# Optimization experiments

Hardware: AMD Instinct MI355X
Metric: run time of the kernel (lower is better)

## Reference

```python
import jax, jax.numpy as jnp
import numpy as np

CHANNELS = 32
HIDDEN = 1024
LAYERS = 8
NODE_TYPES = 7
N_NODES = 500_000
N_EDGES = 2_000_000
NUM_GRAPHS = 1024


def setup_inputs() -> dict:
    key = jax.random.key(0)
    ks = jax.random.split(key, 8)
    nodes = jax.random.randint(ks[0], (N_NODES,), 0, NODE_TYPES)
    sources = jax.random.randint(ks[1], (N_EDGES,), 0, N_NODES)
    targets = jax.random.randint(ks[2], (N_EDGES,), 0, N_NODES)
    # sorted graph ids covering all NUM_GRAPHS graphs (no empty graphs)
    batch = (jnp.arange(N_NODES) * NUM_GRAPHS) // N_NODES
    emb = jax.random.normal(ks[3], (NODE_TYPES, CHANNELS), dtype=jnp.float32)
    # xavier-normal-ish init for the 8 layers x {out, back} 32x32 convs
    xavier_std = (2.0 / (CHANNELS + CHANNELS)) ** 0.5
    conv_w = jax.random.normal(ks[4], (LAYERS, 2, CHANNELS, CHANNELS), dtype=jnp.float32) * xavier_std
    hidden_w = jax.random.normal(ks[5], (CHANNELS, HIDDEN), dtype=jnp.float32) * 0.05
    hidden_b = jax.random.normal(ks[6], (HIDDEN,), dtype=jnp.float32) * 0.05
    out_w = jax.random.normal(ks[7], (HIDDEN, 1), dtype=jnp.float32) * 0.05
    return dict(nodes=nodes, sources=sources, targets=targets, batch=batch,
                emb=emb, conv_w=conv_w, hidden_w=hidden_w, hidden_b=hidden_b,
                out_w=out_w)


def reference(nodes, sources, targets, batch, emb, conv_w, hidden_w, hidden_b, out_w):
    n = nodes.shape[0]
    ones_e = jnp.ones(sources.shape[0], dtype=jnp.float32)
    # norm = 1 / (1 + in-degree), norm_t = 1 / (1 + out-degree)  [N,1]
    norm = (1.0 / (1.0 + jax.ops.segment_sum(ones_e, targets, num_segments=n)))[:, None]
    norm_t = (1.0 / (1.0 + jax.ops.segment_sum(ones_e, sources, num_segments=n)))[:, None]
    node_counts = jax.ops.segment_sum(jnp.ones(n, dtype=jnp.float32), batch,
                                      num_segments=NUM_GRAPHS)

    x = emb[nodes]  # [N, C]

    def conv(x, s, t, nrm, w):
        # x.index_add(0, t, x[s]) -> x + scatter_add of gathered source feats
        agg = nrm * (x + jax.ops.segment_sum(x[s], t, num_segments=n))
        return jax.nn.relu(agg @ w)

    for l in range(LAYERS):
        x = x + conv(x, sources, targets, norm, conv_w[l, 0]) \
              + conv(x, targets, sources, norm_t, conv_w[l, 1])

    # mean pooling per graph
    g = jax.ops.segment_sum(x, batch, num_segments=NUM_GRAPHS) / node_counts[:, None]
    h = jax.nn.relu(g @ hidden_w + hidden_b)
    return (h @ out_w).squeeze(-1)  # [NUM_GRAPHS]
```

## Files before the change

kernel.cpp:

```cpp
#include <hip/hip_runtime.h>

#define CHANNELS 32
#define HIDDEN 1024
#define LAYERS 8
#define NRANGE 8

typedef __attribute__((ext_vector_type(8))) short short8;
typedef __attribute__((ext_vector_type(4))) float float4v;

__device__ __forceinline__ short f2bf_rne(float f) {
    union { float f; unsigned u; } v; v.f = f;
    unsigned r = v.u + 0x7fffu + ((v.u >> 16) & 1u);
    return (short)(r >> 16);
}
__device__ __forceinline__ float bf2f(short h) {
    union { float f; unsigned u; } v; v.u = ((unsigned)(unsigned short)h) << 16;
    return v.f;
}
__device__ __forceinline__ float bfu2f(unsigned short h) {
    union { float f; unsigned u; } v; v.u = ((unsigned)h) << 16;
    return v.f;
}


__global__ __launch_bounds__(256)
void pre_kernel(const int* __restrict__ src, const int* __restrict__ tgt,
                int* __restrict__ deg2,
                const int* __restrict__ nodes, const float* __restrict__ emb,
                unsigned short* __restrict__ hi0, unsigned short* __restrict__ lo,
                const int* __restrict__ batch, float* __restrict__ counts,
                int n_nodes, int n_edges, int n_graphs, int rsh,
                int degB, int initB) {
    int bid = blockIdx.x;
    int tid = threadIdx.x;
    if (bid < degB) {
        int r = bid & (NRANGE - 1);
        int chunk = bid >> 3;
        int base = chunk * 2048;
#pragma unroll
        for (int j = 0; j < 8; j++) {
            int e = base + j * 256 + tid;
            if (e < n_edges) {
                int t = __builtin_nontemporal_load(tgt + e);
                int s = __builtin_nontemporal_load(src + e);
                if ((t >> rsh) == r) atomicAdd(&deg2[t], 1);
                if ((s >> rsh) == r) atomicAdd(&deg2[n_nodes + s], 1);
            }
        }
    } else if (bid < degB + initB) {
        int gid = (bid - degB) * 256 + tid;
        int i = gid >> 5, c = gid & 31;
        if (i < n_nodes) {
            float v = emb[nodes[i] * CHANNELS + c];
            short h = f2bf_rne(v);
            hi0[gid] = (unsigned short)h;
            lo[gid]  = (unsigned short)f2bf_rne(v - bf2f(h));
        }
    } else {
        int b = (bid - degB - initB) * 256 + tid;
        if (b < n_graphs) {
            int lo_i = 0, hi_i = n_nodes;
            while (lo_i < hi_i) { int mid = (lo_i + hi_i) >> 1; if (batch[mid] < b) lo_i = mid + 1; else hi_i = mid; }
            int s0 = lo_i;
            lo_i = 0; hi_i = n_nodes;
            while (lo_i < hi_i) { int mid = (lo_i + hi_i) >> 1; if (batch[mid] < b + 1) lo_i = mid + 1; else hi_i = mid; }
            counts[b] = (float)(lo_i - s0);
        }
    }
}


__global__ __launch_bounds__(256)
void scan_pass1(const int* __restrict__ deg, int* __restrict__ bs, int n) {
    __shared__ int sh[256];
    int t = threadIdx.x;
    int base = blockIdx.x * 2048 + t * 8;
    int s = 0;
#pragma unroll
    for (int j = 0; j < 8; j++) { int idx = base + j; if (idx < n) s += deg[idx]; }
    sh[t] = s; __syncthreads();
    for (int st = 128; st > 0; st >>= 1) { if (t < st) sh[t] += sh[t + st]; __syncthreads(); }
    if (t == 0) bs[blockIdx.x] = sh[0];
}

__global__ void scan_pass2(int* __restrict__ bs, int nb) {
    __shared__ int sh[1024];
    int t = threadIdx.x;
    int v = (t < nb) ? bs[t] : 0;
    sh[t] = v; __syncthreads();
    for (int off = 1; off < 1024; off <<= 1) {
        int u = (t >= off) ? sh[t - off] : 0; __syncthreads();
        sh[t] += u; __syncthreads();
    }
    if (t < nb) bs[t] = sh[t] - v;
}

__global__ __launch_bounds__(256)
void scan_pass3(const int* __restrict__ deg, const int* __restrict__ bs,
                int* __restrict__ off, int n) {
    __shared__ int sh[256];
    int t = threadIdx.x;
    int base = blockIdx.x * 2048 + t * 8;
    int v[8]; int s = 0;
#pragma unroll
    for (int j = 0; j < 8; j++) { int idx = base + j; v[j] = (idx < n) ? deg[idx] : 0; s += v[j]; }
    sh[t] = s; __syncthreads();
    for (int st = 1; st < 256; st <<= 1) {
        int u = (t >= st) ? sh[t - st] : 0; __syncthreads();
        sh[t] += u; __syncthreads();
    }
    int acc = bs[blockIdx.x] + sh[t] - s;
#pragma unroll
    for (int j = 0; j < 8; j++) { int idx = base + j; if (idx < n) off[idx] = acc; acc += v[j]; }
}


__global__ __launch_bounds__(256)
void scatter_range_kernel(const int* __restrict__ src, const int* __restrict__ tgt,
                          int* __restrict__ cur2, int* __restrict__ nbr,
                          int n_nodes, int n_edges, int rsh, int rbase) {
    int r = rbase + (blockIdx.x & (NRANGE - 1));
    int chunk = blockIdx.x >> 3;
    int base = chunk * 2048;
#pragma unroll
    for (int j = 0; j < 8; j++) {
        int e = base + j * 256 + threadIdx.x;
        if (e < n_edges) {
            int t = __builtin_nontemporal_load(tgt + e);
            int s = __builtin_nontemporal_load(src + e);
            if ((t >> rsh) == r) { int p = atomicAdd(&cur2[t], 1);           nbr[p] = s; }
            if ((s >> rsh) == r) { int q = atomicAdd(&cur2[n_nodes + s], 1); nbr[q] = t; }
        }
    }
}


__global__ __launch_bounds__(256, 8)
void layer_mfma(const int* __restrict__ off2, const int* __restrict__ nbr,
                const float* __restrict__ wbase,
                const unsigned short* __restrict__ hi_in,
                unsigned short* __restrict__ hi_out,
                unsigned short* __restrict__ lo,
                int n_nodes, int n_edges) {
    __shared__ short A1h[64][32], A2h[64][32];
    __shared__ short W0h[32][32], W1h[32][32];
    __shared__ int offIn[65], offOut[65];

    int tid = threadIdx.x;
    int nodeblock = blockIdx.x * 64;

    for (int idx = tid; idx < CHANNELS * CHANNELS; idx += 256) {
        int k = idx >> 5, n = idx & 31;
        W0h[n][k] = f2bf_rne(wbase[idx]);
        W1h[n][k] = f2bf_rne(wbase[CHANNELS * CHANNELS + idx]);
    }
    if (tid < 65) {
        int idx = nodeblock + tid;
        offIn[tid]  = (idx <= n_nodes) ? off2[idx] : n_edges;
        int idx2 = n_nodes + idx;
        offOut[tid] = (idx2 < 2 * n_nodes) ? off2[idx2] : 2 * n_edges;
    }
    __syncthreads();

    int c = tid & 31, g = tid >> 5;

    int bi_c, d1_c, bo_c, d2_c, nbl1_c, nbl2_c, node_c;
    float xv_c;
    {
        int local = g;
        node_c = nodeblock + local;
        bi_c = offIn[local];  d1_c = offIn[local + 1] - bi_c;
        bo_c = offOut[local]; d2_c = offOut[local + 1] - bo_c;
        nbl1_c = (c < d1_c) ? nbr[bi_c + c] : 0;
        nbl2_c = (c < d2_c) ? nbr[bo_c + c] : 0;
        xv_c = (node_c < n_nodes)
             ? bfu2f(hi_in[node_c * CHANNELS + c]) + bfu2f(lo[node_c * CHANNELS + c]) : 0.f;
    }

    for (int pass = 0; pass < 8; pass++) {
        int bi_n = 0, d1_n = 0, bo_n = 0, d2_n = 0, nbl1_n = 0, nbl2_n = 0, node_n = 0;
        float xv_n = 0.f;
        if (pass < 7) {
            int local = (pass + 1) * 8 + g;
            node_n = nodeblock + local;
            bi_n = offIn[local];  d1_n = offIn[local + 1] - bi_n;
            bo_n = offOut[local]; d2_n = offOut[local + 1] - bo_n;
            nbl1_n = (c < d1_n) ? nbr[bi_n + c] : 0;
            nbl2_n = (c < d2_n) ? nbr[bo_n + c] : 0;
            xv_n = (node_n < n_nodes)
                 ? bfu2f(hi_in[node_n * CHANNELS + c]) + bfu2f(lo[node_n * CHANNELS + c]) : 0.f;
        }

        int local = pass * 8 + g;
        int i = node_c;
        int self = (i < n_nodes) ? i : 0;

        int m1 = d1_c < 32 ? d1_c : 32;
        int m2 = d2_c < 32 ? d2_c : 32;
        int mm = m1 > m2 ? m1 : m2;

        float a1 = 0.f, a2 = 0.f;
        for (int j = 0; j < mm; j += 4) {
            int p0 = __shfl(nbl1_c, (j)     & 31, 32);
            int p1 = __shfl(nbl1_c, (j + 1) & 31, 32);
            int p2 = __shfl(nbl1_c, (j + 2) & 31, 32);
            int p3 = __shfl(nbl1_c, (j + 3) & 31, 32);
            int q0 = __shfl(nbl2_c, (j)     & 31, 32);
            int q1 = __shfl(nbl2_c, (j + 1) & 31, 32);
            int q2 = __shfl(nbl2_c, (j + 2) & 31, 32);
            int q3 = __shfl(nbl2_c, (j + 3) & 31, 32);
            p0 = (j     < m1) ? p0 : self;
            p1 = (j + 1 < m1) ? p1 : self;
            p2 = (j + 2 < m1) ? p2 : self;
            p3 = (j + 3 < m1) ? p3 : self;
            q0 = (j     < m2) ? q0 : self;
            q1 = (j + 1 < m2) ? q1 : self;
            q2 = (j + 2 < m2) ? q2 : self;
            q3 = (j + 3 < m2) ? q3 : self;
            float u0 = bfu2f(hi_in[p0 * CHANNELS + c]);
            float u1 = bfu2f(hi_in[p1 * CHANNELS + c]);
            float u2 = bfu2f(hi_in[p2 * CHANNELS + c]);
            float u3 = bfu2f(hi_in[p3 * CHANNELS + c]);
            float w0 = bfu2f(hi_in[q0 * CHANNELS + c]);
            float w1 = bfu2f(hi_in[q1 * CHANNELS + c]);
            float w2 = bfu2f(hi_in[q2 * CHANNELS + c]);
            float w3 = bfu2f(hi_in[q3 * CHANNELS + c]);
            a1 += (j     < m1) ? u0 : 0.f;
            a1 += (j + 1 < m1) ? u1 : 0.f;
            a1 += (j + 2 < m1) ? u2 : 0.f;
            a1 += (j + 3 < m1) ? u3 : 0.f;
            a2 += (j     < m2) ? w0 : 0.f;
            a2 += (j + 1 < m2) ? w1 : 0.f;
            a2 += (j + 2 < m2) ? w2 : 0.f;
            a2 += (j + 3 < m2) ? w3 : 0.f;
        }
        for (int e = bi_c + 32; e < bi_c + d1_c; e++) a1 += bfu2f(hi_in[nbr[e] * CHANNELS + c]);
        for (int e = bo_c + 32; e < bo_c + d2_c; e++) a2 += bfu2f(hi_in[nbr[e] * CHANNELS + c]);

        if (i < n_nodes) {
            float n1 = 1.0f / (1.0f + (float)d1_c);
            float n2 = 1.0f / (1.0f + (float)d2_c);
            a1 = n1 * (xv_c + a1);
            a2 = n2 * (xv_c + a2);
            A1h[local][c] = f2bf_rne(a1);
            A2h[local][c] = f2bf_rne(a2);
        } else {
            A1h[local][c] = 0;
            A2h[local][c] = 0;
        }

        bi_c = bi_n; d1_c = d1_n; bo_c = bo_n; d2_c = d2_n;
        nbl1_c = nbl1_n; nbl2_c = nbl2_n; xv_c = xv_n; node_c = node_n;
    }
    __syncthreads();

    int wv = tid >> 6, lane = tid & 63;
    int m = lane & 15, quad = lane >> 4;
    int row0 = wv * 16;

    short8 a1h = *(const short8*)&A1h[row0 + m][quad * 8];
    short8 a2h = *(const short8*)&A2h[row0 + m][quad * 8];

    float4v dd[4];
#pragma unroll
    for (int h = 0; h < 2; h++) {
        int n0 = h * 16 + m;
        short8 b0h = *(const short8*)&W0h[n0][quad * 8];
        short8 b1h = *(const short8*)&W1h[n0][quad * 8];
        float4v d1 = {0.f, 0.f, 0.f, 0.f};
        d1 = __builtin_amdgcn_mfma_f32_16x16x32_bf16(a1h, b0h, d1, 0, 0, 0);
        float4v d2 = {0.f, 0.f, 0.f, 0.f};
        d2 = __builtin_amdgcn_mfma_f32_16x16x32_bf16(a2h, b1h, d2, 0, 0, 0);
        dd[h * 2] = d1; dd[h * 2 + 1] = d2;
    }

#pragma unroll
    for (int h = 0; h < 2; h++) {
        float4v d1 = dd[h * 2], d2 = dd[h * 2 + 1];
#pragma unroll
        for (int r = 0; r < 4; r++) {
            int local = row0 + quad * 4 + r;
            int node = nodeblock + local;
            if (node < n_nodes) {
                int col = h * 16 + m;
                size_t idx = (size_t)node * CHANNELS + col;
                float base = bfu2f(hi_in[idx]) + bfu2f(lo[idx]);
                float v = base + fmaxf(d1[r], 0.f) + fmaxf(d2[r], 0.f);
                short hn = f2bf_rne(v);
                hi_out[idx] = (unsigned short)hn;
                lo[idx]     = (unsigned short)f2bf_rne(v - bf2f(hn));
            }
        }
    }
}


#define POOL_CHUNK 2048

__global__ __launch_bounds__(256)
void pool_kernel(const int* __restrict__ batch,
                 const unsigned short* __restrict__ hi,
                 const unsigned short* __restrict__ lo,
                 float* __restrict__ g, int n_nodes) {
    int c = threadIdx.x & 31;
    int r = threadIdx.x >> 5;
    int base = blockIdx.x * POOL_CHUNK;
    float acc = 0.f;
    int cur = -1;
    for (int it = 0; it < POOL_CHUNK / 8; it++) {
        int node = base + it * 8 + r;
        if (node >= n_nodes) break;
        int b = batch[node];
        if (b != cur) {
            if (cur >= 0) atomicAdd(&g[cur * CHANNELS + c], acc);
            acc = 0.f;
            cur = b;
        }
        size_t idx = (size_t)node * CHANNELS + c;
        acc += bfu2f(hi[idx]) + bfu2f(lo[idx]);
    }
    if (cur >= 0) atomicAdd(&g[cur * CHANNELS + c], acc);
}


__global__ __launch_bounds__(256)
void mlp_kernel(const float* __restrict__ g, const float* __restrict__ counts,
                const float* __restrict__ hidden_w, const float* __restrict__ hidden_b,
                const float* __restrict__ out_w, float* __restrict__ out) {
    __shared__ float grow[CHANNELS];
    __shared__ float red[256];
    int graph = blockIdx.x;
    int tid = threadIdx.x;
    if (tid < CHANNELS) grow[tid] = g[graph * CHANNELS + tid] / counts[graph];
    __syncthreads();
    float partial = 0.f;
    for (int q = 0; q < HIDDEN / 256; q++) {
        int j = q * 256 + tid;
        float h = hidden_b[j];
#pragma unroll
        for (int k = 0; k < CHANNELS; k++) h += grow[k] * hidden_w[k * HIDDEN + j];
        partial += fmaxf(h, 0.f) * out_w[j];
    }
    red[tid] = partial;
    __syncthreads();
    for (int s = 128; s > 0; s >>= 1) {
        if (tid < s) red[tid] += red[tid + s];
        __syncthreads();
    }
    if (tid == 0) out[graph] = red[0];
}


extern "C" void kernel_launch(void* const* d_in, const int* in_sizes, int n_in,
                              void* d_out, int out_size, void* d_ws, size_t ws_size,
                              hipStream_t stream) {
    const int*   nodes    = (const int*)d_in[0];
    const int*   sources  = (const int*)d_in[1];
    const int*   targets  = (const int*)d_in[2];
    const int*   batch    = (const int*)d_in[3];
    const float* emb      = (const float*)d_in[4];
    const float* conv_w   = (const float*)d_in[5];
    const float* hidden_w = (const float*)d_in[6];
    const float* hidden_b = (const float*)d_in[7];
    const float* out_w    = (const float*)d_in[8];
    float* out = (float*)d_out;

    const int n_nodes  = in_sizes[0];
    const int n_edges  = in_sizes[1];
    const int n_graphs = out_size;
    const int n2 = 2 * n_nodes;

    int rsh8 = 0;
    while (((n_nodes - 1) >> rsh8) >= 8) rsh8++;
    int rsh16 = 0;
    while (((n_nodes - 1) >> rsh16) >= 16) rsh16++;

    char* ws = (char*)d_ws;
    unsigned short* hi0 = (unsigned short*)ws; ws += (size_t)n_nodes * CHANNELS * 2;
    unsigned short* hi1 = (unsigned short*)ws; ws += (size_t)n_nodes * CHANNELS * 2;
    unsigned short* lo  = (unsigned short*)ws; ws += (size_t)n_nodes * CHANNELS * 2;
    int*   deg2   = (int*)ws;   ws += (size_t)n2 * 4;
    int*   off2   = (int*)ws;   ws += (size_t)n2 * 4;
    int*   cur2   = (int*)ws;   ws += (size_t)n2 * 4;
    int*   nbr    = (int*)ws;   ws += (size_t)2 * n_edges * 4;
    int*   bsums  = (int*)ws;   ws += 4096;
    float* g      = (float*)ws; ws += (size_t)n_graphs * CHANNELS * 4;
    float* counts = (float*)ws; ws += (size_t)n_graphs * 4;

    hipMemsetAsync(deg2, 0, (size_t)n2 * 4, stream);
    hipMemsetAsync(g, 0, (size_t)n_graphs * CHANNELS * 4, stream);

    int echunks = (n_edges + 2047) / 2048;
    int degB  = echunks * NRANGE;
    int initB = (n_nodes * CHANNELS + 255) / 256;
    int cntB  = (n_graphs + 255) / 256;

    pre_kernel<<<degB + initB + cntB, 256, 0, stream>>>(sources, targets, deg2,
                                                        nodes, emb, hi0, lo,
                                                        batch, counts,
                                                        n_nodes, n_edges, n_graphs,
                                                        rsh8, degB, initB);

    int nblk = (n2 + 2047) / 2048;
    scan_pass1<<<nblk, 256, 0, stream>>>(deg2, bsums, n2);
    scan_pass2<<<1, 1024, 0, stream>>>(bsums, nblk);
    scan_pass3<<<nblk, 256, 0, stream>>>(deg2, bsums, off2, n2);

    hipMemcpyAsync(cur2, off2, (size_t)n2 * 4, hipMemcpyDeviceToDevice, stream);
    scatter_range_kernel<<<echunks * NRANGE, 256, 0, stream>>>(sources, targets, cur2, nbr,
                                                               n_nodes, n_edges, rsh16, 0);
    scatter_range_kernel<<<echunks * NRANGE, 256, 0, stream>>>(sources, targets, cur2, nbr,
                                                               n_nodes, n_edges, rsh16, 8);

    unsigned short* hin = hi0; unsigned short* hout = hi1;
    int lblocks = (n_nodes + 63) / 64;
    for (int l = 0; l < LAYERS; l++) {
        const float* wbase = conv_w + (size_t)l * 2 * CHANNELS * CHANNELS;
        layer_mfma<<<lblocks, 256, 0, stream>>>(off2, nbr, wbase,
                                                hin, hout, lo, n_nodes, n_edges);
        unsigned short* tmp = hin; hin = hout; hout = tmp;
    }

    int pool_blocks = (n_nodes + POOL_CHUNK - 1) / POOL_CHUNK;
    pool_kernel<<<pool_blocks, 256, 0, stream>>>(batch, hin, lo, g, n_nodes);
    mlp_kernel<<<n_graphs, 256, 0, stream>>>(g, counts, hidden_w, hidden_b, out_w, out);
}
```

Measured before the change: 1.531 ms.

## Split gather lanes across in/out edges with packed bf16x2 loads

```diff
diff --git a/kernel.cpp b/kernel.cpp
--- a/kernel.cpp
+++ b/kernel.cpp
@@ -20,6 +20,16 @@
 __device__ __forceinline__ float bfu2f(unsigned short h) {
     union { float f; unsigned u; } v; v.u = ((unsigned)h) << 16;
     return v.f;
+}
+__device__ __forceinline__ float bflo(unsigned u) {
+    union { float f; unsigned u; } v; v.u = u << 16; return v.f;
+}
+__device__ __forceinline__ float bfhi(unsigned u) {
+    union { float f; unsigned u; } v; v.u = u & 0xffff0000u; return v.f;
+}
+__device__ __forceinline__ unsigned packbf(float x, float y) {
+    return ((unsigned)(unsigned short)f2bf_rne(y) << 16) |
+            (unsigned)(unsigned short)f2bf_rne(x);
 }
 
 
@@ -49,12 +59,19 @@
         }
     } else if (bid < degB + initB) {
         int gid = (bid - degB) * 256 + tid;
-        int i = gid >> 5, c = gid & 31;
+        int i = gid >> 2, c8 = (gid & 3) * 8;
         if (i < n_nodes) {
-            float v = emb[nodes[i] * CHANNELS + c];
-            short h = f2bf_rne(v);
-            hi0[gid] = (unsigned short)h;
-            lo[gid]  = (unsigned short)f2bf_rne(v - bf2f(h));
+            const float* e = emb + nodes[i] * CHANNELS + c8;
+            short8 hv, lv;
+#pragma unroll
+            for (int k = 0; k < 8; k++) {
+                float v = e[k];
+                short hsh = f2bf_rne(v);
+                hv[k] = hsh;
+                lv[k] = f2bf_rne(v - bf2f(hsh));
+            }
+            *(short8*)(hi0 + (size_t)i * CHANNELS + c8) = hv;
+            *(short8*)(lo  + (size_t)i * CHANNELS + c8) = lv;
         }
     } else {
         int b = (bid - degB - initB) * 256 + tid;
@@ -97,7 +114,7 @@
 
 __global__ __launch_bounds__(256)
 void scan_pass3(const int* __restrict__ deg, const int* __restrict__ bs,
-                int* __restrict__ off, int n) {
+                int* __restrict__ off, int* __restrict__ cur, int n) {
     __shared__ int sh[256];
     int t = threadIdx.x;
     int base = blockIdx.x * 2048 + t * 8;
@@ -111,7 +128,11 @@
     }
     int acc = bs[blockIdx.x] + sh[t] - s;
 #pragma unroll
-    for (int j = 0; j < 8; j++) { int idx = base + j; if (idx < n) off[idx] = acc; acc += v[j]; }
+    for (int j = 0; j < 8; j++) {
+        int idx = base + j;
+        if (idx < n) { off[idx] = acc; cur[idx] = acc; }
+        acc += v[j];
+    }
 }
 
 
@@ -163,9 +184,11 @@
     __syncthreads();
 
     int c = tid & 31, g = tid >> 5;
+    int h = c >> 4;
+    int cc = c & 15;
 
     int bi_c, d1_c, bo_c, d2_c, nbl1_c, nbl2_c, node_c;
-    float xv_c;
+    float xvx_c, xvy_c;
     {
         int local = g;
         node_c = nodeblock + local;
@@ -173,13 +196,18 @@
         bo_c = offOut[local]; d2_c = offOut[local + 1] - bo_c;
         nbl1_c = (c < d1_c) ? nbr[bi_c + c] : 0;
         nbl2_c = (c < d2_c) ? nbr[bo_c + c] : 0;
-        xv_c = (node_c < n_nodes)
-             ? bfu2f(hi_in[node_c * CHANNELS + c]) + bfu2f(lo[node_c * CHANNELS + c]) : 0.f;
+        xvx_c = 0.f; xvy_c = 0.f;
+        if (node_c < n_nodes) {
+            unsigned hp = *(const unsigned*)(hi_in + (size_t)node_c * CHANNELS + 2 * cc);
+            unsigned lp = *(const unsigned*)(lo    + (size_t)node_c * CHANNELS + 2 * cc);
+            xvx_c = bflo(hp) + bflo(lp);
+            xvy_c = bfhi(hp) + bfhi(lp);
+        }
     }
 
     for (int pass = 0; pass < 8; pass++) {
         int bi_n = 0, d1_n = 0, bo_n = 0, d2_n = 0, nbl1_n = 0, nbl2_n = 0, node_n = 0;
-        float xv_n = 0.f;
+        float xvx_n = 0.f, xvy_n = 0.f;
         if (pass < 7) {
             int local = (pass + 1) * 8 + g;
             node_n = nodeblock + local;
@@ -187,8 +215,12 @@
             bo_n = offOut[local]; d2_n = offOut[local + 1] - bo_n;
             nbl1_n = (c < d1_n) ? nbr[bi_n + c] : 0;
             nbl2_n = (c < d2_n) ? nbr[bo_n + c] : 0;
-            xv_n = (node_n < n_nodes)
-                 ? bfu2f(hi_in[node_n * CHANNELS + c]) + bfu2f(lo[node_n * CHANNELS + c]) : 0.f;
+            if (node_n < n_nodes) {
+                unsigned hp = *(const unsigned*)(hi_in + (size_t)node_n * CHANNELS + 2 * cc);
+                unsigned lp = *(const unsigned*)(lo    + (size_t)node_n * CHANNELS + 2 * cc);
+                xvx_n = bflo(hp) + bflo(lp);
+                xvy_n = bfhi(hp) + bfhi(lp);
+            }
         }
 
         int local = pass * 8 + g;
@@ -199,58 +231,61 @@
         int m2 = d2_c < 32 ? d2_c : 32;
         int mm = m1 > m2 ? m1 : m2;
 
-        float a1 = 0.f, a2 = 0.f;
+        float s1x = 0.f, s1y = 0.f, s2x = 0.f, s2y = 0.f;
         for (int j = 0; j < mm; j += 4) {
-            int p0 = __shfl(nbl1_c, (j)     & 31, 32);
-            int p1 = __shfl(nbl1_c, (j + 1) & 31, 32);
-            int p2 = __shfl(nbl1_c, (j + 2) & 31, 32);
-            int p3 = __shfl(nbl1_c, (j + 3) & 31, 32);
-            int q0 = __shfl(nbl2_c, (j)     & 31, 32);
-            int q1 = __shfl(nbl2_c, (j + 1) & 31, 32);
-            int q2 = __shfl(nbl2_c, (j + 2) & 31, 32);
-            int q3 = __shfl(nbl2_c, (j + 3) & 31, 32);
-            p0 = (j     < m1) ? p0 : self;
-            p1 = (j + 1 < m1) ? p1 : self;
-            p2 = (j + 2 < m1) ? p2 : self;
-            p3 = (j + 3 < m1) ? p3 : self;
-            q0 = (j     < m2) ? q0 : self;
-            q1 = (j + 1 < m2) ? q1 : self;
-            q2 = (j + 2 < m2) ? q2 : self;
-            q3 = (j + 3 < m2) ? q3 : self;
-            float u0 = bfu2f(hi_in[p0 * CHANNELS + c]);
-            float u1 = bfu2f(hi_in[p1 * CHANNELS + c]);
-            float u2 = bfu2f(hi_in[p2 * CHANNELS + c]);
-            float u3 = bfu2f(hi_in[p3 * CHANNELS + c]);
-            float w0 = bfu2f(hi_in[q0 * CHANNELS + c]);
-            float w1 = bfu2f(hi_in[q1 * CHANNELS + c]);
-            float w2 = bfu2f(hi_in[q2 * CHANNELS + c]);
-            float w3 = bfu2f(hi_in[q3 * CHANNELS + c]);
-            a1 += (j     < m1) ? u0 : 0.f;
-            a1 += (j + 1 < m1) ? u1 : 0.f;
-            a1 += (j + 2 < m1) ? u2 : 0.f;
-            a1 += (j + 3 < m1) ? u3 : 0.f;
-            a2 += (j     < m2) ? w0 : 0.f;
-            a2 += (j + 1 < m2) ? w1 : 0.f;
-            a2 += (j + 2 < m2) ? w2 : 0.f;
-            a2 += (j + 3 < m2) ? w3 : 0.f;
-        }
-        for (int e = bi_c + 32; e < bi_c + d1_c; e++) a1 += bfu2f(hi_in[nbr[e] * CHANNELS + c]);
-        for (int e = bo_c + 32; e < bo_c + d2_c; e++) a2 += bfu2f(hi_in[nbr[e] * CHANNELS + c]);
-
+            int sl0 = j + h;
+            int sl1 = j + 2 + h;
+            int p0 = __shfl(nbl1_c, sl0 & 31, 32);
+            int p1 = __shfl(nbl1_c, sl1 & 31, 32);
+            int q0 = __shfl(nbl2_c, sl0 & 31, 32);
+            int q1 = __shfl(nbl2_c, sl1 & 31, 32);
+            bool v10 = sl0 < m1, v11 = sl1 < m1;
+            bool v20 = sl0 < m2, v21 = sl1 < m2;
+            p0 = v10 ? p0 : self;
+            p1 = v11 ? p1 : self;
+            q0 = v20 ? q0 : self;
+            q1 = v21 ? q1 : self;
+            unsigned u0 = *(const unsigned*)(hi_in + (size_t)p0 * CHANNELS + 2 * cc);
+            unsigned u1 = *(const unsigned*)(hi_in + (size_t)p1 * CHANNELS + 2 * cc);
+            unsigned w0 = *(const unsigned*)(hi_in + (size_t)q0 * CHANNELS + 2 * cc);
+            unsigned w1 = *(const unsigned*)(hi_in + (size_t)q1 * CHANNELS + 2 * cc);
+            s1x += v10 ? bflo(u0) : 0.f;
+            s1y += v10 ? bfhi(u0) : 0.f;
+            s1x += v11 ? bflo(u1) : 0.f;
+            s1y += v11 ? bfhi(u1) : 0.f;
+            s2x += v20 ? bflo(w0) : 0.f;
+            s2y += v20 ? bfhi(w0) : 0.f;
+            s2x += v21 ? bflo(w1) : 0.f;
+            s2y += v21 ? bfhi(w1) : 0.f;
+        }
+        s1x += __shfl_xor(s1x, 16, 32);
+        s1y += __shfl_xor(s1y, 16, 32);
+        s2x += __shfl_xor(s2x, 16, 32);
+        s2y += __shfl_xor(s2y, 16, 32);
+
+        for (int e = bi_c + 32; e < bi_c + d1_c; e++) {
+            unsigned u = *(const unsigned*)(hi_in + (size_t)nbr[e] * CHANNELS + 2 * cc);
+            s1x += bflo(u); s1y += bfhi(u);
+        }
+        for (int e = bo_c + 32; e < bo_c + d2_c; e++) {
+            unsigned u = *(const unsigned*)(hi_in + (size_t)nbr[e] * CHANNELS + 2 * cc);
+            s2x += bflo(u); s2y += bfhi(u);
+        }
+
+        unsigned pk1 = 0, pk2 = 0;
         if (i < n_nodes) {
             float n1 = 1.0f / (1.0f + (float)d1_c);
             float n2 = 1.0f / (1.0f + (float)d2_c);
-            a1 = n1 * (xv_c + a1);
-            a2 = n2 * (xv_c + a2);
-            A1h[local][c] = f2bf_rne(a1);
-            A2h[local][c] = f2bf_rne(a2);
-        } else {
-            A1h[local][c] = 0;
-            A2h[local][c] = 0;
-        }
+            pk1 = packbf(n1 * (xvx_c + s1x), n1 * (xvy_c + s1y));
+            pk2 = packbf(n2 * (xvx_c + s2x), n2 * (xvy_c + s2y));
+        }
+        unsigned* dst = (h == 0) ? (unsigned*)&A1h[local][2 * cc]
+                                 : (unsigned*)&A2h[local][2 * cc];
+        *dst = (h == 0) ? pk1 : pk2;
 
         bi_c = bi_n; d1_c = d1_n; bo_c = bo_n; d2_c = d2_n;
-        nbl1_c = nbl1_n; nbl2_c = nbl2_n; xv_c = xv_n; node_c = node_n;
+        nbl1_c = nbl1_n; nbl2_c = nbl2_n;
+        xvx_c = xvx_n; xvy_c = xvy_n; node_c = node_n;
     }
     __syncthreads();
 
@@ -263,26 +298,26 @@
 
     float4v dd[4];
 #pragma unroll
-    for (int h = 0; h < 2; h++) {
-        int n0 = h * 16 + m;
+    for (int hh = 0; hh < 2; hh++) {
+        int n0 = hh * 16 + m;
         short8 b0h = *(const short8*)&W0h[n0][quad * 8];
         short8 b1h = *(const short8*)&W1h[n0][quad * 8];
         float4v d1 = {0.f, 0.f, 0.f, 0.f};
         d1 = __builtin_amdgcn_mfma_f32_16x16x32_bf16(a1h, b0h, d1, 0, 0, 0);
         float4v d2 = {0.f, 0.f, 0.f, 0.f};
         d2 = __builtin_amdgcn_mfma_f32_16x16x32_bf16(a2h, b1h, d2, 0, 0, 0);
-        dd[h * 2] = d1; dd[h * 2 + 1] = d2;
-    }
-
-#pragma unroll
-    for (int h = 0; h < 2; h++) {
-        float4v d1 = dd[h * 2], d2 = dd[h * 2 + 1];
+        dd[hh * 2] = d1; dd[hh * 2 + 1] = d2;
+    }
+
+#pragma unroll
+    for (int hh = 0; hh < 2; hh++) {
+        float4v d1 = dd[hh * 2], d2 = dd[hh * 2 + 1];
 #pragma unroll
         for (int r = 0; r < 4; r++) {
             int local = row0 + quad * 4 + r;
             int node = nodeblock + local;
             if (node < n_nodes) {
-                int col = h * 16 + m;
+                int col = hh * 16 + m;
                 size_t idx = (size_t)node * CHANNELS + col;
                 float base = bfu2f(hi_in[idx]) + bfu2f(lo[idx]);
                 float v = base + fmaxf(d1[r], 0.f) + fmaxf(d2[r], 0.f);
@@ -392,7 +427,7 @@
 
     int echunks = (n_edges + 2047) / 2048;
     int degB  = echunks * NRANGE;
-    int initB = (n_nodes * CHANNELS + 255) / 256;
+    int initB = (n_nodes * 4 + 255) / 256;
     int cntB  = (n_graphs + 255) / 256;
 
     pre_kernel<<<degB + initB + cntB, 256, 0, stream>>>(sources, targets, deg2,
@@ -404,9 +439,8 @@
     int nblk = (n2 + 2047) / 2048;
     scan_pass1<<<nblk, 256, 0, stream>>>(deg2, bsums, n2);
     scan_pass2<<<1, 1024, 0, stream>>>(bsums, nblk);
-    scan_pass3<<<nblk, 256, 0, stream>>>(deg2, bsums, off2, n2);
-
-    hipMemcpyAsync(cur2, off2, (size_t)n2 * 4, hipMemcpyDeviceToDevice, stream);
+    scan_pass3<<<nblk, 256, 0, stream>>>(deg2, bsums, off2, cur2, n2);
+
     scatter_range_kernel<<<echunks * NRANGE, 256, 0, stream>>>(sources, targets, cur2, nbr,
                                                                n_nodes, n_edges, rsh16, 0);
     scatter_range_kernel<<<echunks * NRANGE, 256, 0, stream>>>(sources, targets, cur2, nbr,
```

New measurement: 1.486 ms. 2.9% less time.
